# Optimization experiments

Hardware: AMD Instinct MI355X
Metric: run time of the kernel (lower is better)

## Reference

```python
import jax, jax.numpy as jnp
import numpy as np

N = 8192   # nodes per graph batch
D = 128    # node_feat_dim
E = 131072 # edges per graph batch
B = 64     # graphs per batch


def _linear_init(k, fin, fout):
    s = 1.0 / np.sqrt(fin)
    kw, kb = jax.random.split(k)
    W = jax.random.uniform(kw, (fin, fout), jnp.float32, -s, s)
    b = jax.random.uniform(kb, (fout,), jnp.float32, -s, s)
    return W, b


def setup_inputs() -> dict:
    key = jax.random.key(0)
    ks = jax.random.split(key, 10)
    x1 = jax.random.normal(ks[0], (N, D), jnp.float32)
    x2 = jax.random.normal(ks[1], (N, D), jnp.float32)
    edge_index1 = jax.random.randint(ks[2], (2, E), 0, N)
    edge_index2 = jax.random.randint(ks[3], (2, E), 0, N)
    # block-contiguous graph ids; every graph id present on both sides
    batch = jnp.arange(N, dtype=jnp.int32) // (N // B)
    mW1, mb1 = _linear_init(ks[4], 2 * D, 512)
    mW2, mb2 = _linear_init(ks[5], 512, 256)  # 256 == 2*D (update_net constraint)
    uW1, ub1 = _linear_init(ks[6], 4 * D, 512)
    uW2, ub2 = _linear_init(ks[7], 512, 256)
    uW3, ub3 = _linear_init(ks[8], 256, D)
    return dict(x1=x1, edge_index1=edge_index1, batch1=batch,
                x2=x2, edge_index2=edge_index2, batch2=batch,
                mW1=mW1, mb1=mb1, mW2=mW2, mb2=mb2,
                uW1=uW1, ub1=ub1, uW2=uW2, ub2=ub2, uW3=uW3, ub3=ub3)


def _message_aggr(x, edge_index, mW1, mb1, mW2, mb2):
    tgt, src = edge_index[0], edge_index[1]
    inp = jnp.concatenate([x[src], x[tgt]], axis=-1)          # [E, 2D]
    msg = jax.nn.relu(inp @ mW1 + mb1) @ mW2 + mb2            # [E, 2D]
    return jax.ops.segment_sum(msg, tgt, num_segments=x.shape[0])


def _cross_attention(x1, batch1, x2, batch2):
    scores = x1 @ x2.T                                        # [N1, N2]
    mask = batch1[:, None] == batch2[None, :]
    scores = jnp.where(mask, scores, -jnp.inf)
    att1 = x1 - jax.nn.softmax(scores, axis=1) @ x2
    att2 = x2 - jax.nn.softmax(scores, axis=0).T @ x1
    return att1, att2


def _node_update(x, messages, attentions, uW1, ub1, uW2, ub2, uW3, ub3):
    u = jnp.concatenate([messages, attentions, x], axis=-1)   # [N, 4D]
    h = jax.nn.relu(u @ uW1 + ub1)
    h = jax.nn.relu(h @ uW2 + ub2)
    return x + h @ uW3 + ub3                                  # residual update


def reference(x1, edge_index1, batch1, x2, edge_index2, batch2,
              mW1, mb1, mW2, mb2, uW1, ub1, uW2, ub2, uW3, ub3):
    m1 = _message_aggr(x1, edge_index1, mW1, mb1, mW2, mb2)
    m2 = _message_aggr(x2, edge_index2, mW1, mb1, mW2, mb2)
    a1, a2 = _cross_attention(x1, batch1, x2, batch2)
    new_x1 = _node_update(x1, m1, a1, uW1, ub1, uW2, ub2, uW3, ub3)
    new_x2 = _node_update(x2, m2, a2, uW1, ub1, uW2, ub2, uW3, ub3)
    return new_x1, new_x2
```

## Files before the change

### kernel.cpp

```cpp
#include <hip/hip_runtime.h>
#include <stdint.h>


typedef unsigned short u16;
typedef __bf16 bf16x8 __attribute__((ext_vector_type(8)));
typedef float f32x4 __attribute__((ext_vector_type(4)));

#define NN 8192
#define DD 128
#define EE 131072
#define GS 128
#define NG 64

__device__ __forceinline__ float bf2f(u16 u){
  return __uint_as_float(((uint32_t)u) << 16);
}
__device__ __forceinline__ u16 f2bf(float f){
  uint32_t x = __float_as_uint(f);
  return (u16)((x + 0x7fffu + ((x >> 16) & 1u)) >> 16);
}
__device__ __forceinline__ void gload16(const u16* g, u16* l){
  __builtin_amdgcn_global_load_lds(
      (const __attribute__((address_space(1))) uint32_t*)(uintptr_t)g,
      (__attribute__((address_space(3))) uint32_t*)(uintptr_t)l, 16, 0, 0);
}
__device__ __forceinline__ void gfence(){
  asm volatile("s_waitcnt vmcnt(0)" ::: "memory");
  __builtin_amdgcn_s_barrier();
  __builtin_amdgcn_sched_barrier(0);
}

template<bool RELU, bool DEGBIAS, bool RES, typename OT>
__device__ __forceinline__ void gemm_body(
    const u16* __restrict__ A, int lda,
    const u16* __restrict__ Wt, const float* __restrict__ bias,
    const int* __restrict__ deg,
    const float* __restrict__ res1, const float* __restrict__ res2,
    OT* __restrict__ out, int ldc, int K, int bx, int by,
    u16* __restrict__ sh, int t)
{
  u16* As0 = sh;         u16* Bs0 = sh + 4096;
  u16* As1 = sh + 8192;  u16* Bs1 = sh + 12288;
  const int brow = by << 7, bcol = bx << 7;
  const int w = t >> 6, lane = t & 63;
  const int rb = (w >> 1) << 6, cb = (w & 1) << 6;
  const int lr = lane & 15, lq = lane >> 4;

  f32x4 acc[4][4];
  #pragma unroll
  for (int i = 0; i < 4; i++)
    #pragma unroll
    for (int j = 0; j < 4; j++) acc[i][j] = (f32x4){0.f, 0.f, 0.f, 0.f};

  const int s0 = t, s1 = t + 256;
  const int sw0 = (((s0 & 3) ^ ((s0 >> 2) & 3)) << 3);
  const int sw1 = (((s1 & 3) ^ ((s1 >> 2) & 3)) << 3);
  const u16* Ag0 = A  + (size_t)(brow + (s0 >> 2)) * lda + sw0;
  const u16* Ag1 = A  + (size_t)(brow + (s1 >> 2)) * lda + sw1;
  const u16* Bg0 = Wt + (size_t)(bcol + (s0 >> 2)) * K   + sw0;
  const u16* Bg1 = Wt + (size_t)(bcol + (s1 >> 2)) * K   + sw1;
  const int d0 = s0 << 3, d1 = s1 << 3;

  auto stage = [&](int kb, u16* Al, u16* Bl){
    gload16(Ag0 + kb, Al + d0);
    gload16(Ag1 + kb, Al + d1);
    gload16(Bg0 + kb, Bl + d0);
    gload16(Bg1 + kb, Bl + d1);
  };
  const int swr = ((lq ^ (lr & 3)) << 3);
  auto compute = [&](const u16* Asb, const u16* Bsb){
    bf16x8 af[4], bfr[4];
    #pragma unroll
    for (int mi = 0; mi < 4; mi++)
      af[mi] = *(const bf16x8*)&Asb[(rb + mi * 16 + lr) * 32 + swr];
    #pragma unroll
    for (int ni = 0; ni < 4; ni++)
      bfr[ni] = *(const bf16x8*)&Bsb[(cb + ni * 16 + lr) * 32 + swr];
    #pragma unroll
    for (int mi = 0; mi < 4; mi++)
      #pragma unroll
      for (int ni = 0; ni < 4; ni++)
        acc[mi][ni] = __builtin_amdgcn_mfma_f32_16x16x32_bf16(af[mi], bfr[ni], acc[mi][ni], 0, 0, 0);
  };

  stage(0, As0, Bs0);
  gfence();
  for (int kb = 0; kb < K; kb += 64){
    if (kb + 32 < K) stage(kb + 32, As1, Bs1);
    compute(As0, Bs0);
    gfence();
    if (kb + 64 < K) stage(kb + 64, As0, Bs0);
    compute(As1, Bs1);
    gfence();
  }

  #pragma unroll
  for (int mi = 0; mi < 4; mi++)
    #pragma unroll
    for (int ni = 0; ni < 4; ni++)
      #pragma unroll
      for (int rr = 0; rr < 4; rr++){
        int grow = brow + rb + mi * 16 + lq * 4 + rr;
        int gcol = bcol + cb + ni * 16 + lr;
        float v = acc[mi][ni][rr];
        if (bias) v += DEGBIAS ? (float)deg[grow] * bias[gcol] : bias[gcol];
        if constexpr (RELU) v = fmaxf(v, 0.f);
        if constexpr (RES){
          const float* rp = (grow < NN) ? res1 : res2;
          v += rp[(size_t)(grow & (NN - 1)) * ldc + gcol];
        }
        if constexpr (sizeof(OT) == 2) out[(size_t)grow * ldc + gcol] = (OT)f2bf(v);
        else                           out[(size_t)grow * ldc + gcol] = (OT)v;
      }
}

__global__ __launch_bounds__(256)
void pre_k(const float* __restrict__ mW1, const float* __restrict__ mb1,
           const float* __restrict__ mW2, const float* __restrict__ uW1,
           const float* __restrict__ uW2, const float* __restrict__ uW3,
           const float* __restrict__ x1, const float* __restrict__ x2,
           const int* __restrict__ ei1, const int* __restrict__ ei2,
           u16* __restrict__ WtPQ, float* __restrict__ bPQ,
           u16* __restrict__ Wtm2, u16* __restrict__ Wtu1,
           u16* __restrict__ Wtu2, u16* __restrict__ Wtu3,
           u16* __restrict__ xb, u16* __restrict__ xt,
           u16* __restrict__ U, int* __restrict__ deg)
{
  __shared__ u16 T[8704];
  int b = blockIdx.x, t = threadIdx.x;
  if (b < 2692){
    if (b < 512){
      int idx = b * 256 + t; int c = idx >> 7, k = idx & 127;
      int row = (c < 512) ? k : 128 + k;
      WtPQ[idx] = f2bf(mW1[(size_t)row * 512 + (c & 511)]);
    } else if (b < 1024){
      int idx = (b - 512) * 256 + t; int c = idx >> 9, k = idx & 511;
      Wtm2[idx] = f2bf(mW2[(size_t)k * 256 + c]);
    } else if (b < 2048){
      int idx = (b - 1024) * 256 + t; int c = idx >> 9, k = idx & 511;
      Wtu1[idx] = f2bf(uW1[(size_t)k * 512 + c]);
    } else if (b < 2560){
      int idx = (b - 2048) * 256 + t; int c = idx >> 9, k = idx & 511;
      Wtu2[idx] = f2bf(uW2[(size_t)k * 256 + c]);
    } else if (b < 2688){
      int idx = (b - 2560) * 256 + t; int c = idx >> 8, k = idx & 255;
      Wtu3[idx] = f2bf(uW3[(size_t)k * 128 + c]);
    } else {
      int idx = (b - 2688) * 256 + t;
      bPQ[idx] = (idx < 512) ? 0.f : mb1[idx - 512];
    }
  } else if (b < 4740){
    int a = b - 2692;
    int side = a >> 10, blk = a & 1023;
    const float* x = side ? x2 : x1;
    int i4 = blk * 256 + t;
    float4 v = *(const float4*)&x[(size_t)i4 * 4];
    uint2 pk;
    pk.x = (uint32_t)f2bf(v.x) | ((uint32_t)f2bf(v.y) << 16);
    pk.y = (uint32_t)f2bf(v.z) | ((uint32_t)f2bf(v.w) << 16);
    *(uint2*)&xb[(size_t)side * NN * DD + (size_t)i4 * 4] = pk;
    int n = i4 >> 5, d = (i4 << 2) & 127;
    *(uint2*)&U[((size_t)side * NN + n) * 512 + 384 + d] = pk;
  } else if (b < 4996){
    int a = b - 4740;
    int side = a >> 7, blk = a & 127;
    const float* x = side ? x2 : x1;
    u16* dst = xt + (size_t)side * DD * NN;
    const int n0 = blk * 64;
    #pragma unroll
    for (int i = 0; i < 8; i++){
      int s = i * 256 + t;
      int r = s >> 5, c4 = (s & 31) << 2;
      float4 v = *(const float4*)&x[(size_t)(n0 + r) * DD + c4];
      uint2 pk;
      pk.x = (uint32_t)f2bf(v.x) | ((uint32_t)f2bf(v.y) << 16);
      pk.y = (uint32_t)f2bf(v.z) | ((uint32_t)f2bf(v.w) << 16);
      *(uint2*)&T[r * 136 + c4] = pk;
    }
    __syncthreads();
    #pragma unroll
    for (int i = 0; i < 8; i++){
      int s = i * 256 + t;
      int d = s >> 4, n4 = (s & 15) << 2;
      uint32_t a0 = T[(n4 + 0) * 136 + d];
      uint32_t a1 = T[(n4 + 1) * 136 + d];
      uint32_t a2 = T[(n4 + 2) * 136 + d];
      uint32_t a3 = T[(n4 + 3) * 136 + d];
      uint2 pk; pk.x = a0 | (a1 << 16); pk.y = a2 | (a3 << 16);
      *(uint2*)(dst + (size_t)d * NN + n0 + n4) = pk;
    }
  } else {
    int a = b - 4996;
    int side = a >> 9, blk = a & 511;
    const int* ei = side ? ei2 : ei1;
    int e = blk * 256 + t;
    atomicAdd(&deg[side * NN + ei[e]], 1);
  }
}

__global__ __launch_bounds__(256)
void scan_k(const int* __restrict__ deg,
            int* __restrict__ offs1, int* __restrict__ cur1,
            int* __restrict__ offs2, int* __restrict__ cur2){
  const int* d = deg + blockIdx.x * NN;
  int* offs = blockIdx.x ? offs2 : offs1;
  int* cur  = blockIdx.x ? cur2  : cur1;
  __shared__ int part[256];
  const int t = threadIdx.x;
  const int base = t * 32;
  int loc[32];
  int s = 0;
  #pragma unroll
  for (int i = 0; i < 32; i++){ loc[i] = s; s += d[base + i]; }
  part[t] = s;
  __syncthreads();
  for (int off = 1; off < 256; off <<= 1){
    int v = (t >= off) ? part[t - off] : 0;
    __syncthreads();
    part[t] += v;
    __syncthreads();
  }
  int pre = (t == 0) ? 0 : part[t - 1];
  #pragma unroll
  for (int i = 0; i < 32; i++){
    int o = pre + loc[i];
    offs[base + i] = o;
    cur[base + i]  = o;
  }
  if (t == 255) offs[NN] = part[255];
}

__global__ __launch_bounds__(256)
void mid_k(const u16* __restrict__ xb, const u16* __restrict__ WtPQ,
           const float* __restrict__ bPQ, u16* __restrict__ PQ,
           const int* __restrict__ ei1, const int* __restrict__ ei2,
           int* __restrict__ cur1, int* __restrict__ cur2,
           int* __restrict__ srt1, int* __restrict__ srt2)
{
  __shared__ u16 sh[16384];
  const int b = blockIdx.x, t = threadIdx.x;
  if (b < 1024){
    gemm_body<false,false,false,u16>(xb, 128, WtPQ, bPQ, nullptr, nullptr, nullptr,
                                     PQ, 1024, 128, b >> 7, b & 127, sh, t);
  } else {
    int a = b - 1024;
    int side = a >> 9, blk = a & 511;
    const int* ei = side ? ei2 : ei1;
    int* cur = side ? cur2 : cur1;
    int* srt = side ? srt2 : srt1;
    int e = blk * 256 + t;
    int tgt = ei[e], src = ei[EE + e];
    int p = atomicAdd(&cur[tgt], 1);
    srt[p] = src;
  }
}

__global__ __launch_bounds__(256)
void gather_k(const int* __restrict__ offs1, const int* __restrict__ srt1,
              const int* __restrict__ offs2, const int* __restrict__ srt2,
              const u16* __restrict__ PQ, u16* __restrict__ S)
{
  const int side = blockIdx.y;
  const int* offs = side ? offs2 : offs1;
  const int* srt  = side ? srt2  : srt1;
  const u16* base = PQ + (size_t)side * NN * 1024;
  u16* Sb = S + (size_t)side * NN * 512;

  const int node = (blockIdx.x << 2) + (threadIdx.x >> 6);
  const int lane = threadIdx.x & 63;
  const int beg = offs[node], end = offs[node + 1];

  uint4 qv = *(const uint4*)(base + (size_t)node * 1024 + 512 + (lane << 3));
  float q[8];
  {
    uint32_t qw[4] = {qv.x, qv.y, qv.z, qv.w};
    #pragma unroll
    for (int i = 0; i < 4; i++){
      q[i * 2]     = bf2f((u16)(qw[i] & 0xffffu));
      q[i * 2 + 1] = bf2f((u16)(qw[i] >> 16));
    }
  }
  float acc[8] = {0.f,0.f,0.f,0.f,0.f,0.f,0.f,0.f};

  int e = beg;
  for (; e + 7 < end; e += 8){
    int sx[8];
    #pragma unroll
    for (int i = 0; i < 8; i++) sx[i] = srt[e + i];
    uint4 pv[8];
    #pragma unroll
    for (int i = 0; i < 8; i++)
      pv[i] = *(const uint4*)(base + (size_t)sx[i] * 1024 + (lane << 3));
    #pragma unroll
    for (int i = 0; i < 8; i++){
      uint32_t w0[4] = {pv[i].x, pv[i].y, pv[i].z, pv[i].w};
      #pragma unroll
      for (int j = 0; j < 4; j++){
        acc[j*2]   += fmaxf(bf2f((u16)(w0[j] & 0xffffu)) + q[j*2],   0.f);
        acc[j*2+1] += fmaxf(bf2f((u16)(w0[j] >> 16))     + q[j*2+1], 0.f);
      }
    }
  }
  for (; e + 3 < end; e += 4){
    int sx[4];
    #pragma unroll
    for (int i = 0; i < 4; i++) sx[i] = srt[e + i];
    uint4 pv[4];
    #pragma unroll
    for (int i = 0; i < 4; i++)
      pv[i] = *(const uint4*)(base + (size_t)sx[i] * 1024 + (lane << 3));
    #pragma unroll
    for (int i = 0; i < 4; i++){
      uint32_t w0[4] = {pv[i].x, pv[i].y, pv[i].z, pv[i].w};
      #pragma unroll
      for (int j = 0; j < 4; j++){
        acc[j*2]   += fmaxf(bf2f((u16)(w0[j] & 0xffffu)) + q[j*2],   0.f);
        acc[j*2+1] += fmaxf(bf2f((u16)(w0[j] >> 16))     + q[j*2+1], 0.f);
      }
    }
  }
  for (; e < end; e++){
    int sA = srt[e];
    uint4 pA = *(const uint4*)(base + (size_t)sA * 1024 + (lane << 3));
    uint32_t aw[4] = {pA.x, pA.y, pA.z, pA.w};
    #pragma unroll
    for (int i = 0; i < 4; i++){
      acc[i*2]   += fmaxf(bf2f((u16)(aw[i] & 0xffffu)) + q[i*2],   0.f);
      acc[i*2+1] += fmaxf(bf2f((u16)(aw[i] >> 16))     + q[i*2+1], 0.f);
    }
  }
  uint4 pk;
  pk.x = (uint32_t)f2bf(acc[0]) | ((uint32_t)f2bf(acc[1]) << 16);
  pk.y = (uint32_t)f2bf(acc[2]) | ((uint32_t)f2bf(acc[3]) << 16);
  pk.z = (uint32_t)f2bf(acc[4]) | ((uint32_t)f2bf(acc[5]) << 16);
  pk.w = (uint32_t)f2bf(acc[6]) | ((uint32_t)f2bf(acc[7]) << 16);
  *(uint4*)(Sb + (size_t)node * 512 + (lane << 3)) = pk;
}

__global__ __launch_bounds__(256)
void msgattn_k(const u16* __restrict__ S, const u16* __restrict__ Wtm2,
               const float* __restrict__ mb2, const int* __restrict__ deg,
               const u16* __restrict__ xb, const u16* __restrict__ xt,
               u16* __restrict__ U)
{
  __shared__ u16 sh[26112];
  const int b = blockIdx.x, t = threadIdx.x;
  if (b < 256){
    gemm_body<false,true,false,u16>(S, 512, Wtm2, mb2, deg, nullptr, nullptr,
                                    U, 512, 512, b >> 7, b & 127, sh, t);
    return;
  }
  const int a = b - 256;
  const int side = a >> 7;
  const int g = a & 63, h = (a >> 6) & 1;
  const u16* Xa = xb + (size_t)side * NN * DD;
  const u16* Xb = xb + (size_t)(1 - side) * NN * DD;
  const u16* Xt = xt + (size_t)(1 - side) * DD * NN;
  u16* Uside = U + (size_t)side * NN * 512;

  u16* XaS = sh;
  u16* XbS = sh + 8704;

  const int w = t >> 6, lane = t & 63;
  const int lr = lane & 15, lq = lane >> 4;

  {
    const u16* sa = Xa + ((size_t)g * GS + h * 64) * DD;
    #pragma unroll
    for (int i = 0; i < 4; i++){
      int s = i * 256 + t; int r = s >> 4, c8 = (s & 15) << 3;
      *(uint4*)&XaS[r * 136 + c8] = *(const uint4*)(sa + (size_t)r * DD + c8);
    }
    const u16* sb = Xb + (size_t)g * GS * DD;
    #pragma unroll
    for (int i = 0; i < 8; i++){
      int s = i * 256 + t; int r = s >> 4, c8 = (s & 15) << 3;
      *(uint4*)&XbS[r * 136 + c8] = *(const uint4*)(sb + (size_t)r * DD + c8);
    }
  }
  __syncthreads();

  f32x4 sc[8];
  #pragma unroll
  for (int ct = 0; ct < 8; ct++) sc[ct] = (f32x4){0.f, 0.f, 0.f, 0.f};
  #pragma unroll
  for (int kb = 0; kb < 4; kb++){
    bf16x8 aa = *(const bf16x8*)&XaS[(w * 16 + lr) * 136 + kb * 32 + (lq << 3)];
    #pragma unroll
    for (int ct = 0; ct < 8; ct++){
      bf16x8 bb = *(const bf16x8*)&XbS[(ct * 16 + lr) * 136 + kb * 32 + (lq << 3)];
      sc[ct] = __builtin_amdgcn_mfma_f32_16x16x32_bf16(aa, bb, sc[ct], 0, 0, 0);
    }
  }
  float inv[4];
  #pragma unroll
  for (int rr = 0; rr < 4; rr++){
    float m = sc[0][rr];
    #pragma unroll
    for (int ct = 1; ct < 8; ct++) m = fmaxf(m, sc[ct][rr]);
    #pragma unroll
    for (int sh_ = 1; sh_ < 16; sh_ <<= 1) m = fmaxf(m, __shfl_xor(m, sh_, 64));
    float s = 0.f;
    #pragma unroll
    for (int ct = 0; ct < 8; ct++){
      float e = __expf(sc[ct][rr] - m);
      sc[ct][rr] = e; s += e;
    }
    #pragma unroll
    for (int sh_ = 1; sh_ < 16; sh_ <<= 1) s += __shfl_xor(s, sh_, 64);
    inv[rr] = 1.f / s;
  }
  #pragma unroll
  for (int ct = 0; ct < 8; ct++)
    #pragma unroll
    for (int rr = 0; rr < 4; rr++)
      XaS[(w * 16 + lq * 4 + rr) * 136 + ct * 16 + lr] = f2bf(sc[ct][rr] * inv[rr]);
  __syncthreads();

  f32x4 o[8];
  #pragma unroll
  for (int ct = 0; ct < 8; ct++) o[ct] = (f32x4){0.f, 0.f, 0.f, 0.f};
  #pragma unroll
  for (int kb = 0; kb < 4; kb++){
    bf16x8 aa = *(const bf16x8*)&XaS[(w * 16 + lr) * 136 + kb * 32 + (lq << 3)];
    #pragma unroll
    for (int ct = 0; ct < 8; ct++){
      bf16x8 bb = *(const bf16x8*)(Xt + (size_t)(ct * 16 + lr) * NN + g * GS + kb * 32 + (lq << 3));
      o[ct] = __builtin_amdgcn_mfma_f32_16x16x32_bf16(aa, bb, o[ct], 0, 0, 0);
    }
  }
  const u16* XaG = Xa + ((size_t)g * GS + h * 64) * DD;
  #pragma unroll
  for (int ct = 0; ct < 8; ct++)
    #pragma unroll
    for (int rr = 0; rr < 4; rr++){
      int row = w * 16 + lq * 4 + rr, col = ct * 16 + lr;
      float xa = bf2f(XaG[(size_t)row * DD + col]);
      Uside[((size_t)g * GS + h * 64 + row) * 512 + 256 + col] = f2bf(xa - o[ct][rr]);
    }
}

__global__ __launch_bounds__(512)
void upd_k(const u16* __restrict__ U,
           const u16* __restrict__ Wtu1, const float* __restrict__ ub1,
           const u16* __restrict__ Wtu2, const float* __restrict__ ub2,
           const u16* __restrict__ Wtu3, const float* __restrict__ ub3,
           const float* __restrict__ x1, const float* __restrict__ x2,
           float* __restrict__ out)
{
  __shared__ u16 sh[70656];
  u16* H1s  = sh;
  u16* H2s  = sh + 33280;
  u16* Bst0 = sh + 50176;
  u16* Bst1 = sh + 58368;
  u16* Ast0 = sh + 66560;
  u16* Ast1 = sh + 68608;

  const int t = threadIdx.x;
  const int w = t >> 6, lane = t & 63;
  const int wr = w >> 2, wc = w & 3;
  const int lr = lane & 15, lq = lane >> 4;
  const int r0 = blockIdx.x << 6;

  const int sA = t;
  const int rA = sA >> 2;
  const int swA = (((sA & 3) ^ (rA & 3)) << 3);
  const int sB0 = t, sB1 = t + 512;
  const int cB0 = sB0 >> 2, cB1 = sB1 >> 2;
  const int swB0 = (((sB0 & 3) ^ (cB0 & 3)) << 3);
  const int swB1 = (((sB1 & 3) ^ (cB1 & 3)) << 3);
  const int swr = ((lq ^ (lr & 3)) << 3);

  f32x4 acc[2][4];
  auto zacc = [&](){
    #pragma unroll
    for (int i = 0; i < 2; i++)
      #pragma unroll
      for (int j = 0; j < 4; j++) acc[i][j] = (f32x4){0.f, 0.f, 0.f, 0.f};
  };

  for (int hN = 0; hN < 2; hN++){
    zacc();
    auto stA = [&](int kb, u16* dst){
      if (t < 256) gload16(U + (size_t)(r0 + rA) * 512 + kb + swA, dst + sA * 8);
    };
    auto stB = [&](int kb, u16* dst){
      gload16(Wtu1 + (size_t)(hN * 256 + cB0) * 512 + kb + swB0, dst + sB0 * 8);
      gload16(Wtu1 + (size_t)(hN * 256 + cB1) * 512 + kb + swB1, dst + sB1 * 8);
    };
    auto comp = [&](const u16* Asb, const u16* Bsb){
      bf16x8 af[2], bfv[4];
      #pragma unroll
      for (int mi = 0; mi < 2; mi++)
        af[mi] = *(const bf16x8*)&Asb[(wr * 32 + mi * 16 + lr) * 32 + swr];
      #pragma unroll
      for (int ct = 0; ct < 4; ct++)
        bfv[ct] = *(const bf16x8*)&Bsb[(wc * 64 + ct * 16 + lr) * 32 + swr];
      #pragma unroll
      for (int mi = 0; mi < 2; mi++)
        #pragma unroll
        for (int ct = 0; ct < 4; ct++)
          acc[mi][ct] = __builtin_amdgcn_mfma_f32_16x16x32_bf16(af[mi], bfv[ct], acc[mi][ct], 0, 0, 0);
    };
    stA(0, Ast0); stB(0, Bst0);
    gfence();
    for (int kb = 0; kb < 512; kb += 64){
      if (kb + 32 < 512){ stA(kb + 32, Ast1); stB(kb + 32, Bst1); }
      comp(Ast0, Bst0);
      gfence();
      if (kb + 64 < 512){ stA(kb + 64, Ast0); stB(kb + 64, Bst0); }
      comp(Ast1, Bst1);
      gfence();
    }
    #pragma unroll
    for (int mi = 0; mi < 2; mi++)
      #pragma unroll
      for (int ct = 0; ct < 4; ct++)
        #pragma unroll
        for (int rr = 0; rr < 4; rr++){
          int row = wr * 32 + mi * 16 + lq * 4 + rr;
          int col = wc * 64 + ct * 16 + lr;
          float v = acc[mi][ct][rr] + ub1[hN * 256 + col];
          H1s[row * 520 + hN * 256 + col] = f2bf(fmaxf(v, 0.f));
        }
  }
  __syncthreads();

  zacc();
  {
    auto stB = [&](int kb, u16* dst){
      gload16(Wtu2 + (size_t)cB0 * 512 + kb + swB0, dst + sB0 * 8);
      gload16(Wtu2 + (size_t)cB1 * 512 + kb + swB1, dst + sB1 * 8);
    };
    auto comp = [&](int kb, const u16* Bsb){
      bf16x8 af[2], bfv[4];
      #pragma unroll
      for (int mi = 0; mi < 2; mi++)
        af[mi] = *(const bf16x8*)&H1s[(wr * 32 + mi * 16 + lr) * 520 + kb + (lq << 3)];
      #pragma unroll
      for (int ct = 0; ct < 4; ct++)
        bfv[ct] = *(const bf16x8*)&Bsb[(wc * 64 + ct * 16 + lr) * 32 + swr];
      #pragma unroll
      for (int mi = 0; mi < 2; mi++)
        #pragma unroll
        for (int ct = 0; ct < 4; ct++)
          acc[mi][ct] = __builtin_amdgcn_mfma_f32_16x16x32_bf16(af[mi], bfv[ct], acc[mi][ct], 0, 0, 0);
    };
    stB(0, Bst0);
    gfence();
    for (int kb = 0; kb < 512; kb += 64){
      if (kb + 32 < 512) stB(kb + 32, Bst1);
      comp(kb, Bst0);
      gfence();
      if (kb + 64 < 512) stB(kb + 64, Bst0);
      comp(kb + 32, Bst1);
      gfence();
    }
    #pragma unroll
    for (int mi = 0; mi < 2; mi++)
      #pragma unroll
      for (int ct = 0; ct < 4; ct++)
        #pragma unroll
        for (int rr = 0; rr < 4; rr++){
          int row = wr * 32 + mi * 16 + lq * 4 + rr;
          int col = wc * 64 + ct * 16 + lr;
          H2s[row * 264 + col] = f2bf(fmaxf(acc[mi][ct][rr] + ub2[col], 0.f));
        }
  }
  __syncthreads();

  zacc();
  {
    auto stB = [&](int kb, u16* dst){
      gload16(Wtu3 + (size_t)cB0 * 256 + kb + swB0, dst + sB0 * 8);
    };
    auto comp = [&](int kb, const u16* Bsb){
      bf16x8 af[2], bfv[2];
      #pragma unroll
      for (int mi = 0; mi < 2; mi++)
        af[mi] = *(const bf16x8*)&H2s[(wr * 32 + mi * 16 + lr) * 264 + kb + (lq << 3)];
      #pragma unroll
      for (int ct = 0; ct < 2; ct++)
        bfv[ct] = *(const bf16x8*)&Bsb[(wc * 32 + ct * 16 + lr) * 32 + swr];
      #pragma unroll
      for (int mi = 0; mi < 2; mi++)
        #pragma unroll
        for (int ct = 0; ct < 2; ct++)
          acc[mi][ct] = __builtin_amdgcn_mfma_f32_16x16x32_bf16(af[mi], bfv[ct], acc[mi][ct], 0, 0, 0);
    };
    stB(0, Bst0);
    gfence();
    for (int kb = 0; kb < 256; kb += 64){
      if (kb + 32 < 256) stB(kb + 32, Bst1);
      comp(kb, Bst0);
      gfence();
      if (kb + 64 < 256) stB(kb + 64, Bst0);
      comp(kb + 32, Bst1);
      gfence();
    }
    #pragma unroll
    for (int mi = 0; mi < 2; mi++)
      #pragma unroll
      for (int ct = 0; ct < 2; ct++)
        #pragma unroll
        for (int rr = 0; rr < 4; rr++){
          int row = wr * 32 + mi * 16 + lq * 4 + rr;
          int col = wc * 32 + ct * 16 + lr;
          int grow = r0 + row;
          const float* rp = (grow < NN) ? x1 : x2;
          float v = acc[mi][ct][rr] + ub3[col]
                  + rp[(size_t)(grow & (NN - 1)) * 128 + col];
          out[(size_t)grow * 128 + col] = v;
        }
  }
}

extern "C" void kernel_launch(void* const* d_in, const int* in_sizes, int n_in,
                              void* d_out, int out_size, void* d_ws, size_t ws_size,
                              hipStream_t stream)
{
  const float* x1  = (const float*)d_in[0];
  const int*   ei1 = (const int*)  d_in[1];
  const float* x2  = (const float*)d_in[3];
  const int*   ei2 = (const int*)  d_in[4];
  const float* mW1 = (const float*)d_in[6];
  const float* mb1 = (const float*)d_in[7];
  const float* mW2 = (const float*)d_in[8];
  const float* mb2 = (const float*)d_in[9];
  const float* uW1 = (const float*)d_in[10];
  const float* ub1 = (const float*)d_in[11];
  const float* uW2 = (const float*)d_in[12];
  const float* ub2 = (const float*)d_in[13];
  const float* uW3 = (const float*)d_in[14];
  const float* ub3 = (const float*)d_in[15];
  float* out = (float*)d_out;

  char* w = (char*)d_ws;
  auto alloc = [&](size_t b){ char* p = w; w += (b + 255) & ~(size_t)255; return p; };
  u16*  S    = (u16*)alloc((size_t)2 * NN * 512 * 2);
  u16*  PQ   = (u16*)alloc((size_t)2 * NN * 1024 * 2);
  u16*  xb   = (u16*)alloc((size_t)2 * NN * DD * 2);
  u16*  xt   = (u16*)alloc((size_t)2 * DD * NN * 2);
  u16*  U    = (u16*)alloc((size_t)2 * NN * 512 * 2);
  int*  deg  = (int*)alloc((size_t)2 * NN * 4);
  int*  offs1 = (int*)alloc((NN + 1) * 4);
  int*  offs2 = (int*)alloc((NN + 1) * 4);
  int*  cur1  = (int*)alloc(NN * 4);
  int*  cur2  = (int*)alloc(NN * 4);
  int*  srt1  = (int*)alloc((size_t)EE * 4);
  int*  srt2  = (int*)alloc((size_t)EE * 4);
  u16*  WtPQ = (u16*)alloc(1024 * 128 * 2);
  float* bPQ = (float*)alloc(1024 * 4);
  u16*  Wtm2 = (u16*)alloc(256 * 512 * 2);
  u16*  Wtu1 = (u16*)alloc(512 * 512 * 2);
  u16*  Wtu2 = (u16*)alloc(256 * 512 * 2);
  u16*  Wtu3 = (u16*)alloc(128 * 256 * 2);

  hipMemsetAsync(deg, 0, (size_t)2 * NN * 4, stream);

  pre_k<<<4996 + 1024, 256, 0, stream>>>(
      mW1, mb1, mW2, uW1, uW2, uW3, x1, x2, ei1, ei2,
      WtPQ, bPQ, Wtm2, Wtu1, Wtu2, Wtu3, xb, xt, U, deg);

  scan_k<<<2, 256, 0, stream>>>(deg, offs1, cur1, offs2, cur2);

  mid_k<<<2048, 256, 0, stream>>>(xb, WtPQ, bPQ, PQ, ei1, ei2,
                                  cur1, cur2, srt1, srt2);

  gather_k<<<dim3(NN / 4, 2), 256, 0, stream>>>(offs1, srt1, offs2, srt2, PQ, S);

  msgattn_k<<<512, 256, 0, stream>>>(S, Wtm2, mb2, deg, xb, xt, U);

  upd_k<<<256, 512, 0, stream>>>(U, Wtu1, ub1, Wtu2, ub2, Wtu3, ub3,
                                 x1, x2, out);
}
```

Before: 238.8 us.

## Pipeline GEMM loads with partial vmcnt waits and register-load update A operand

Replaces the full-drain wait before each barrier with a partial vmcnt wait, so the prefetch of the next K-slice stays in flight while the current slice is computed. The PQ projection GEMM (K=128) becomes a dedicated single-stage kernel that loads the whole K extent into swizzled LDS at once. The update MLP's first layer now reads its A operand straight from global memory into registers instead of staging it through LDS. The aim is to hide memory latency and cut barrier stalls, at the cost of more LDS for the PQ block and uncoalesced, non-LDS global reads of U.

```diff
diff --git a/kernel.cpp b/kernel.cpp
--- a/kernel.cpp
+++ b/kernel.cpp
@@ -24,18 +24,25 @@
       (const __attribute__((address_space(1))) uint32_t*)(uintptr_t)g,
       (__attribute__((address_space(3))) uint32_t*)(uintptr_t)l, 16, 0, 0);
 }
-__device__ __forceinline__ void gfence(){
-  asm volatile("s_waitcnt vmcnt(0)" ::: "memory");
+template<int N>
+__device__ __forceinline__ void wbar(){
+  if constexpr (N == 0)      asm volatile("s_waitcnt vmcnt(0)" ::: "memory");
+  else if constexpr (N == 1) asm volatile("s_waitcnt vmcnt(1)" ::: "memory");
+  else if constexpr (N == 2) asm volatile("s_waitcnt vmcnt(2)" ::: "memory");
+  else if constexpr (N == 4) asm volatile("s_waitcnt vmcnt(4)" ::: "memory");
   __builtin_amdgcn_s_barrier();
   __builtin_amdgcn_sched_barrier(0);
 }
-
-template<bool RELU, bool DEGBIAS, bool RES, typename OT>
+__device__ __forceinline__ void bar(){
+  __builtin_amdgcn_s_barrier();
+  __builtin_amdgcn_sched_barrier(0);
+}
+
+template<bool DEGBIAS, typename OT>
 __device__ __forceinline__ void gemm_body(
     const u16* __restrict__ A, int lda,
     const u16* __restrict__ Wt, const float* __restrict__ bias,
     const int* __restrict__ deg,
-    const float* __restrict__ res1, const float* __restrict__ res2,
     OT* __restrict__ out, int ldc, int K, int bx, int by,
     u16* __restrict__ sh, int t)
 {
@@ -84,14 +91,21 @@
   };
 
   stage(0, As0, Bs0);
-  gfence();
-  for (int kb = 0; kb < K; kb += 64){
-    if (kb + 32 < K) stage(kb + 32, As1, Bs1);
+  const int half = K >> 6;
+  for (int i2 = 0; i2 < half; i2++){
+    const int kb = i2 << 6;
+    stage(kb + 32, As1, Bs1);
+    wbar<4>();
     compute(As0, Bs0);
-    gfence();
-    if (kb + 64 < K) stage(kb + 64, As0, Bs0);
+    bar();
+    if (i2 + 1 < half){
+      stage(kb + 64, As0, Bs0);
+      wbar<4>();
+    } else {
+      wbar<0>();
+    }
     compute(As1, Bs1);
-    gfence();
+    bar();
   }
 
   #pragma unroll
@@ -104,13 +118,67 @@
         int gcol = bcol + cb + ni * 16 + lr;
         float v = acc[mi][ni][rr];
         if (bias) v += DEGBIAS ? (float)deg[grow] * bias[gcol] : bias[gcol];
-        if constexpr (RELU) v = fmaxf(v, 0.f);
-        if constexpr (RES){
-          const float* rp = (grow < NN) ? res1 : res2;
-          v += rp[(size_t)(grow & (NN - 1)) * ldc + gcol];
-        }
-        if constexpr (sizeof(OT) == 2) out[(size_t)grow * ldc + gcol] = (OT)f2bf(v);
-        else                           out[(size_t)grow * ldc + gcol] = (OT)v;
+        out[(size_t)grow * ldc + gcol] = (OT)f2bf(v);
+      }
+}
+
+__device__ __forceinline__ void pq_gemm(
+    const u16* __restrict__ A, const u16* __restrict__ Wt,
+    const float* __restrict__ bias, u16* __restrict__ out,
+    int bx, int by, u16* __restrict__ sh, int t)
+{
+  u16* As = sh;
+  u16* Bs = sh + 16384;
+  const int brow = by << 7, bcol = bx << 7;
+  const int w = t >> 6, lane = t & 63;
+  const int rb = (w >> 1) << 6, cb = (w & 1) << 6;
+  const int lr = lane & 15, lq = lane >> 4;
+
+  #pragma unroll
+  for (int i = 0; i < 8; i++){
+    int sg = i * 256 + t;
+    int r = sg >> 4, p = sg & 15;
+    int l = p ^ (r & 7);
+    gload16(A  + (size_t)(brow + r) * 128 + (l << 3), As + sg * 8);
+    gload16(Wt + (size_t)(bcol + r) * 128 + (l << 3), Bs + sg * 8);
+  }
+  wbar<0>();
+
+  f32x4 acc[4][4];
+  #pragma unroll
+  for (int i = 0; i < 4; i++)
+    #pragma unroll
+    for (int j = 0; j < 4; j++) acc[i][j] = (f32x4){0.f, 0.f, 0.f, 0.f};
+
+  #pragma unroll
+  for (int kb = 0; kb < 4; kb++){
+    bf16x8 af[4], bfr[4];
+    #pragma unroll
+    for (int mi = 0; mi < 4; mi++){
+      int row = rb + mi * 16 + lr;
+      af[mi] = *(const bf16x8*)&As[(row << 7) + ((((kb << 2) | lq) ^ (row & 7)) << 3)];
+    }
+    #pragma unroll
+    for (int ni = 0; ni < 4; ni++){
+      int row = cb + ni * 16 + lr;
+      bfr[ni] = *(const bf16x8*)&Bs[(row << 7) + ((((kb << 2) | lq) ^ (row & 7)) << 3)];
+    }
+    #pragma unroll
+    for (int mi = 0; mi < 4; mi++)
+      #pragma unroll
+      for (int ni = 0; ni < 4; ni++)
+        acc[mi][ni] = __builtin_amdgcn_mfma_f32_16x16x32_bf16(af[mi], bfr[ni], acc[mi][ni], 0, 0, 0);
+  }
+
+  #pragma unroll
+  for (int mi = 0; mi < 4; mi++)
+    #pragma unroll
+    for (int ni = 0; ni < 4; ni++)
+      #pragma unroll
+      for (int rr = 0; rr < 4; rr++){
+        int grow = brow + rb + mi * 16 + lq * 4 + rr;
+        int gcol = bcol + cb + ni * 16 + lr;
+        out[(size_t)grow * 1024 + gcol] = f2bf(acc[mi][ni][rr] + bias[gcol]);
       }
 }
 
@@ -237,11 +305,10 @@
            int* __restrict__ cur1, int* __restrict__ cur2,
            int* __restrict__ srt1, int* __restrict__ srt2)
 {
-  __shared__ u16 sh[16384];
+  __shared__ u16 sh[32768];
   const int b = blockIdx.x, t = threadIdx.x;
   if (b < 1024){
-    gemm_body<false,false,false,u16>(xb, 128, WtPQ, bPQ, nullptr, nullptr, nullptr,
-                                     PQ, 1024, 128, b >> 7, b & 127, sh, t);
+    pq_gemm(xb, WtPQ, bPQ, PQ, b >> 7, b & 127, sh, t);
   } else {
     int a = b - 1024;
     int side = a >> 9, blk = a & 511;
@@ -346,8 +413,8 @@
   __shared__ u16 sh[26112];
   const int b = blockIdx.x, t = threadIdx.x;
   if (b < 256){
-    gemm_body<false,true,false,u16>(S, 512, Wtm2, mb2, deg, nullptr, nullptr,
-                                    U, 512, 512, b >> 7, b & 127, sh, t);
+    gemm_body<true,u16>(S, 512, Wtm2, mb2, deg,
+                        U, 512, 512, b >> 7, b & 127, sh, t);
     return;
   }
   const int a = b - 256;
@@ -448,13 +515,11 @@
            const float* __restrict__ x1, const float* __restrict__ x2,
            float* __restrict__ out)
 {
-  __shared__ u16 sh[70656];
+  __shared__ u16 sh[66560];
   u16* H1s  = sh;
   u16* H2s  = sh + 33280;
   u16* Bst0 = sh + 50176;
   u16* Bst1 = sh + 58368;
-  u16* Ast0 = sh + 66560;
-  u16* Ast1 = sh + 68608;
 
   const int t = threadIdx.x;
   const int w = t >> 6, lane = t & 63;
@@ -462,9 +527,6 @@
   const int lr = lane & 15, lq = lane >> 4;
   const int r0 = blockIdx.x << 6;
 
-  const int sA = t;
-  const int rA = sA >> 2;
-  const int swA = (((sA & 3) ^ (rA & 3)) << 3);
   const int sB0 = t, sB1 = t + 512;
   const int cB0 = sB0 >> 2, cB1 = sB1 >> 2;
   const int swB0 = (((sB0 & 3) ^ (cB0 & 3)) << 3);
@@ -479,38 +541,45 @@
       for (int j = 0; j < 4; j++) acc[i][j] = (f32x4){0.f, 0.f, 0.f, 0.f};
   };
 
+  bf16x8 afA[2], afB[2];
+  auto ldA = [&](int kb, bf16x8 (&af)[2]){
+    #pragma unroll
+    for (int mi = 0; mi < 2; mi++)
+      af[mi] = *(const bf16x8*)&U[(size_t)(r0 + wr * 32 + mi * 16 + lr) * 512 + kb + (lq << 3)];
+  };
+  auto compA = [&](const bf16x8 (&af)[2], const u16* Bsb){
+    bf16x8 bfv[4];
+    #pragma unroll
+    for (int ct = 0; ct < 4; ct++)
+      bfv[ct] = *(const bf16x8*)&Bsb[(wc * 64 + ct * 16 + lr) * 32 + swr];
+    #pragma unroll
+    for (int mi = 0; mi < 2; mi++)
+      #pragma unroll
+      for (int ct = 0; ct < 4; ct++)
+        acc[mi][ct] = __builtin_amdgcn_mfma_f32_16x16x32_bf16(af[mi], bfv[ct], acc[mi][ct], 0, 0, 0);
+  };
   for (int hN = 0; hN < 2; hN++){
     zacc();
-    auto stA = [&](int kb, u16* dst){
-      if (t < 256) gload16(U + (size_t)(r0 + rA) * 512 + kb + swA, dst + sA * 8);
-    };
     auto stB = [&](int kb, u16* dst){
       gload16(Wtu1 + (size_t)(hN * 256 + cB0) * 512 + kb + swB0, dst + sB0 * 8);
       gload16(Wtu1 + (size_t)(hN * 256 + cB1) * 512 + kb + swB1, dst + sB1 * 8);
     };
-    auto comp = [&](const u16* Asb, const u16* Bsb){
-      bf16x8 af[2], bfv[4];
-      #pragma unroll
-      for (int mi = 0; mi < 2; mi++)
-        af[mi] = *(const bf16x8*)&Asb[(wr * 32 + mi * 16 + lr) * 32 + swr];
-      #pragma unroll
-      for (int ct = 0; ct < 4; ct++)
-        bfv[ct] = *(const bf16x8*)&Bsb[(wc * 64 + ct * 16 + lr) * 32 + swr];
-      #pragma unroll
-      for (int mi = 0; mi < 2; mi++)
-        #pragma unroll
-        for (int ct = 0; ct < 4; ct++)
-          acc[mi][ct] = __builtin_amdgcn_mfma_f32_16x16x32_bf16(af[mi], bfv[ct], acc[mi][ct], 0, 0, 0);
-    };
-    stA(0, Ast0); stB(0, Bst0);
-    gfence();
-    for (int kb = 0; kb < 512; kb += 64){
-      if (kb + 32 < 512){ stA(kb + 32, Ast1); stB(kb + 32, Bst1); }
-      comp(Ast0, Bst0);
-      gfence();
-      if (kb + 64 < 512){ stA(kb + 64, Ast0); stB(kb + 64, Bst0); }
-      comp(Ast1, Bst1);
-      gfence();
+    stB(0, Bst0);
+    ldA(0, afA);
+    for (int i2 = 0; i2 < 8; i2++){
+      const int kb = i2 << 6;
+      stB(kb + 32, Bst1); ldA(kb + 32, afB);
+      wbar<4>();
+      compA(afA, Bst0);
+      bar();
+      if (i2 < 7){
+        stB(kb + 64, Bst0); ldA(kb + 64, afA);
+        wbar<4>();
+      } else {
+        wbar<0>();
+      }
+      compA(afB, Bst1);
+      bar();
     }
     #pragma unroll
     for (int mi = 0; mi < 2; mi++)
@@ -547,14 +616,20 @@
           acc[mi][ct] = __builtin_amdgcn_mfma_f32_16x16x32_bf16(af[mi], bfv[ct], acc[mi][ct], 0, 0, 0);
     };
     stB(0, Bst0);
-    gfence();
-    for (int kb = 0; kb < 512; kb += 64){
-      if (kb + 32 < 512) stB(kb + 32, Bst1);
+    for (int i2 = 0; i2 < 8; i2++){
+      const int kb = i2 << 6;
+      stB(kb + 32, Bst1);
+      wbar<2>();
       comp(kb, Bst0);
-      gfence();
-      if (kb + 64 < 512) stB(kb + 64, Bst0);
+      bar();
+      if (i2 < 7){
+        stB(kb + 64, Bst0);
+        wbar<2>();
+      } else {
+        wbar<0>();
+      }
       comp(kb + 32, Bst1);
-      gfence();
+      bar();
     }
     #pragma unroll
     for (int mi = 0; mi < 2; mi++)
@@ -589,14 +664,20 @@
           acc[mi][ct] = __builtin_amdgcn_mfma_f32_16x16x32_bf16(af[mi], bfv[ct], acc[mi][ct], 0, 0, 0);
     };
     stB(0, Bst0);
-    gfence();
-    for (int kb = 0; kb < 256; kb += 64){
-      if (kb + 32 < 256) stB(kb + 32, Bst1);
+    for (int i2 = 0; i2 < 4; i2++){
+      const int kb = i2 << 6;
+      stB(kb + 32, Bst1);
+      wbar<1>();
       comp(kb, Bst0);
-      gfence();
-      if (kb + 64 < 256) stB(kb + 64, Bst0);
+      bar();
+      if (i2 < 3){
+        stB(kb + 64, Bst0);
+        wbar<1>();
+      } else {
+        wbar<0>();
+      }
       comp(kb + 32, Bst1);
-      gfence();
+      bar();
     }
     #pragma unroll
     for (int mi = 0; mi < 2; mi++)
```

After: 222.2 us. -6.9%, faster.
